# Kernel tuning notes

Hardware: AMD Instinct MI355X
Metric: run time of the kernel (lower is better)

The kernel has to match this reference:

```python
import jax, jax.numpy as jnp
import numpy as np

DT = 0.001  # euler step size (module default dt)
T = 2000    # num_timesteps
N_IN = 8192
N_OUT = 4096


def setup_inputs() -> dict:
    key = jax.random.key(0)
    k_x, k_w = jax.random.split(key)
    x = jax.random.normal(k_x, (T, N_IN), dtype=jnp.float32)
    # module initializes weight.data.uniform_(-0.1, 0.1)
    weight = jax.random.uniform(k_w, (N_OUT, N_IN), dtype=jnp.float32, minval=-0.1, maxval=0.1)
    ones = jnp.ones((N_OUT,), dtype=jnp.float32)
    # default_lif_parameters broadcast to per-neuron vectors (constant_lif_parameters)
    return {
        "x": x,
        "weight": weight,
        "v_th": ones * 75.0,
        "v_rest": ones * 50.0,
        "v_reset": ones * 30.0,
        "t_ref": ones * 0.001,
        "tau": ones * 2.0,
    }


def reference(x, weight, v_th, v_rest, v_reset, t_ref, tau):
    # lif_input[t] = x[t] @ weight.T  -> [T, N_OUT]
    lif_input = x @ weight.T

    def step(carry, inp):
        v, refrac = carry
        # leak toward v_rest
        v = v - DT * tau * (v - v_rest)
        # integrate input only when not refractory
        v = v + jnp.where(refrac == 0, inp, jnp.zeros_like(inp))
        # count down refractory period
        refrac = jnp.where(refrac > 0, refrac - DT, jnp.zeros_like(refrac))
        # heavyside spike
        spike = (v - v_th >= 0).astype(v.dtype)
        sb = spike > 0
        # reset: refractory period and membrane potential
        refrac = jnp.where(sb, t_ref, refrac)
        v = jnp.where(sb, v_reset, v)
        return (v, refrac), spike

    v0 = v_rest.astype(x.dtype)               # v[0] = v_rest
    refrac0 = jnp.zeros_like(v0)
    # torch loop runs i = 1 .. T-1 consuming lif_input[i]
    _, spikes = jax.lax.scan(step, (v0, refrac0), lif_input[1:])
    s0 = jnp.zeros((1, spikes.shape[1]), dtype=spikes.dtype)  # s[0] stays zero
    return jnp.concatenate([s0, spikes], axis=0)  # [T, N_OUT]
```

## Files before the change

kernel.cpp:

```cpp
#include <hip/hip_runtime.h>
#include <hip/hip_bf16.h>


#define T_STEPS 2000
#define NIN_K   8192
#define NOUT_N  4096
#define MPAD    2048

typedef __attribute__((ext_vector_type(8))) _Float16 half8;
typedef __attribute__((ext_vector_type(4))) float f32x4;

#define GLL16(g, l)                                                              \
    __builtin_amdgcn_global_load_lds(                                            \
        (const __attribute__((address_space(1))) void*)(g),                      \
        (__attribute__((address_space(3))) void*)(l), 16, 0, 0)

__global__ __launch_bounds__(256) void split_f32(const float* __restrict__ src,
                                                 _Float16* __restrict__ hi,
                                                 _Float16* __restrict__ lo,
                                                 size_t n_valid) {
    const size_t i8 = (size_t)(blockIdx.x * 256u + threadIdx.x) * 8;
    float vv[8];
    if (i8 < n_valid) {
        float4 v0 = *(const float4*)(src + i8);
        float4 v1 = *(const float4*)(src + i8 + 4);
        vv[0] = v0.x; vv[1] = v0.y; vv[2] = v0.z; vv[3] = v0.w;
        vv[4] = v1.x; vv[5] = v1.y; vv[6] = v1.z; vv[7] = v1.w;
    } else {
#pragma unroll
        for (int j = 0; j < 8; ++j) vv[j] = 0.f;
    }
    half8 h8, l8;
#pragma unroll
    for (int j = 0; j < 8; ++j) {
        _Float16 h = (_Float16)vv[j];
        float r = __fsub_rn(vv[j], (float)h);
        h8[j] = h;
        l8[j] = (_Float16)(r * 4096.0f);
    }
    *(half8*)(hi + i8) = h8;
    *(half8*)(lo + i8) = l8;
}

__global__ __launch_bounds__(256, 2) void gemm_f16x2(const _Float16* __restrict__ A0,
                                                     const _Float16* __restrict__ A1,
                                                     const _Float16* __restrict__ B0,
                                                     const _Float16* __restrict__ B1,
                                                     float* __restrict__ C) {
    __shared__ _Float16 lds[4][128 * 64];

    const int tid  = threadIdx.x;
    const int wave = tid >> 6;
    const int lane = tid & 63;
    const int bm = blockIdx.y * 128;
    const int bn = blockIdx.x * 128;
    const int wm = (wave >> 1) * 64;
    const int wn = (wave & 1) * 64;

    const int srow = tid >> 3;
    const int skswz = ((tid & 7) ^ (srow & 7)) * 8;

    f32x4 acc0[4][4], acc1[4][4];
#pragma unroll
    for (int i = 0; i < 4; ++i)
#pragma unroll
        for (int j = 0; j < 4; ++j) {
            acc0[i][j] = (f32x4){0.f, 0.f, 0.f, 0.f};
            acc1[i][j] = (f32x4){0.f, 0.f, 0.f, 0.f};
        }

    const int quad = lane >> 4;
    const int l16  = lane & 15;

    for (int k0 = 0; k0 < NIN_K; k0 += 64) {
        __syncthreads();
#pragma unroll
        for (int c = 0; c < 4; ++c) {
            const size_t ga = (size_t)(bm + c * 32 + srow) * NIN_K + k0 + skswz;
            const size_t gb = (size_t)(bn + c * 32 + srow) * NIN_K + k0 + skswz;
            const int base = (c * 32 + wave * 8) * 64;
            GLL16(A0 + ga, &lds[0][base]);
            GLL16(A1 + ga, &lds[1][base]);
            GLL16(B0 + gb, &lds[2][base]);
            GLL16(B1 + gb, &lds[3][base]);
        }
        __syncthreads();

#pragma unroll
        for (int ks = 0; ks < 2; ++ks) {
            half8 b0f[4], b1f[4];
#pragma unroll
            for (int j = 0; j < 4; ++j) {
                const int row = wn + j * 16 + l16;
                const int off = row * 64 + ((ks * 4 + quad) ^ (row & 7)) * 8;
                b0f[j] = *(const half8*)&lds[2][off];
                b1f[j] = *(const half8*)&lds[3][off];
            }
#pragma unroll
            for (int i = 0; i < 4; ++i) {
                const int row = wm + i * 16 + l16;
                const int off = row * 64 + ((ks * 4 + quad) ^ (row & 7)) * 8;
                const half8 a0f = *(const half8*)&lds[0][off];
                const half8 a1f = *(const half8*)&lds[1][off];
#pragma unroll
                for (int j = 0; j < 4; ++j) {
                    acc0[i][j] = __builtin_amdgcn_mfma_f32_16x16x32_f16(a0f, b0f[j], acc0[i][j], 0, 0, 0);
                    acc1[i][j] = __builtin_amdgcn_mfma_f32_16x16x32_f16(a0f, b1f[j], acc1[i][j], 0, 0, 0);
                    acc1[i][j] = __builtin_amdgcn_mfma_f32_16x16x32_f16(a1f, b0f[j], acc1[i][j], 0, 0, 0);
                }
            }
        }
    }

    const float s = 1.0f / 4096.0f;
#pragma unroll
    for (int i = 0; i < 4; ++i)
#pragma unroll
        for (int j = 0; j < 4; ++j) {
            const int m = bm + wm + i * 16 + quad * 4;
            const int n = bn + wn + j * 16 + l16;
            float* cp = C + (size_t)m * NOUT_N + n;
#pragma unroll
            for (int r = 0; r < 4; ++r)
                cp[(size_t)r * NOUT_N] = __fmaf_rn(acc1[i][j][r], s, acc0[i][j][r]);
        }
}

#define BM 64
#define BN 64
#define BK 16
#define PAD 4
__global__ __launch_bounds__(256) void gemm_bt(const float* __restrict__ A,
                                               const float* __restrict__ B,
                                               float* __restrict__ C,
                                               int M, int N, int K) {
    __shared__ float As[BK][BM + PAD];
    __shared__ float Bs[BK][BN + PAD];
    const int bm = blockIdx.y * BM, bn = blockIdx.x * BN;
    const int tid = threadIdx.x;
    const int tx = tid & 15, ty = tid >> 4;
    const int lrow = tid >> 2, lk = (tid & 3) * 4;
    float acc[4][4];
#pragma unroll
    for (int i = 0; i < 4; ++i)
#pragma unroll
        for (int j = 0; j < 4; ++j) acc[i][j] = 0.0f;
    for (int k0 = 0; k0 < K; k0 += BK) {
        const int am = bm + lrow;
        float4 av = (am < M) ? *(const float4*)(A + (size_t)am * K + k0 + lk)
                             : make_float4(0.f, 0.f, 0.f, 0.f);
        As[lk + 0][lrow] = av.x; As[lk + 1][lrow] = av.y;
        As[lk + 2][lrow] = av.z; As[lk + 3][lrow] = av.w;
        float4 bv = *(const float4*)(B + (size_t)(bn + lrow) * K + k0 + lk);
        Bs[lk + 0][lrow] = bv.x; Bs[lk + 1][lrow] = bv.y;
        Bs[lk + 2][lrow] = bv.z; Bs[lk + 3][lrow] = bv.w;
        __syncthreads();
#pragma unroll
        for (int k = 0; k < BK; ++k) {
            float a[4], b[4];
#pragma unroll
            for (int i = 0; i < 4; ++i) a[i] = As[k][ty * 4 + i];
#pragma unroll
            for (int j = 0; j < 4; ++j) b[j] = Bs[k][tx * 4 + j];
#pragma unroll
            for (int i = 0; i < 4; ++i)
#pragma unroll
                for (int j = 0; j < 4; ++j) acc[i][j] += a[i] * b[j];
        }
        __syncthreads();
    }
#pragma unroll
    for (int i = 0; i < 4; ++i) {
        const int m = bm + ty * 4 + i;
        if (m < M) {
            float* cp = C + (size_t)m * N + bn + tx * 4;
#pragma unroll
            for (int j = 0; j < 4; ++j) cp[j] = acc[i][j];
        }
    }
}

__global__ void zero_rows(float* __restrict__ p, size_t n) {
    const size_t i = (size_t)blockIdx.x * 256 + threadIdx.x;
    if (i < n) p[i] = 0.0f;
}

__global__ __launch_bounds__(64) void lif_scan(const float* __restrict__ inp,
                                               const float* __restrict__ v_th_p,
                                               const float* __restrict__ v_rest_p,
                                               const float* __restrict__ v_reset_p,
                                               const float* __restrict__ t_ref_p,
                                               const float* __restrict__ tau_p,
                                               float* __restrict__ out) {
    const int lane = threadIdx.x;
    const int j = blockIdx.x * 64 + lane;

    const float vth = v_th_p[j], vrest = v_rest_p[j], vres = v_reset_p[j];
    const float tref = t_ref_p[j];
    const float cleak = __fmul_rn(0.001f, tau_p[j]);
    float v = vrest, refrac = 0.0f;
    out[j] = 0.0f;

    const float* plv = inp + (size_t)1 * NOUT_N + j;
    float* pst = out + (size_t)1 * NOUT_N + j;

    float p00, p01, p02, p03, p04, p05, p06, p07, p08, p09, p10, p11, p12, p13, p14, p15;
    float p16, p17, p18, p19, p20, p21, p22, p23, p24, p25, p26, p27, p28, p29, p30, p31;

#define LDP(PD)                                                                   \
    asm volatile("global_load_dword %0, %1, off" : "=v"(PD) : "v"(plv) : "memory"); \
    plv += NOUT_N;

#define STEPA(PD, WSTR)                                                           \
    {                                                                             \
        asm volatile(WSTR : "+v"(PD)::"memory");                                  \
        const float in = PD;                                                      \
        const float dd = __fmul_rn(cleak, __fsub_rn(v, vrest));                   \
        v = __fsub_rn(v, dd);                                                     \
        v = (refrac == 0.0f) ? __fadd_rn(v, in) : v;                              \
        refrac = (refrac > 0.0f) ? (refrac - 0.001f) : 0.0f;                      \
        const bool s = (__fsub_rn(v, vth) >= 0.0f);                               \
        const float spk = s ? 1.0f : 0.0f;                                        \
        asm volatile("global_store_dword %0, %1, off" ::"v"(pst), "v"(spk)        \
                     : "memory");                                                 \
        pst += NOUT_N;                                                            \
        asm volatile("global_load_dword %0, %1, off" : "=v"(PD) : "v"(plv)        \
                     : "memory");                                                 \
        plv += NOUT_N;                                                            \
        refrac = s ? tref : refrac;                                               \
        v = s ? vres : v;                                                         \
    }

#define GROUP32(WSTR)                                                             \
    STEPA(p00, WSTR) STEPA(p01, WSTR) STEPA(p02, WSTR) STEPA(p03, WSTR)           \
    STEPA(p04, WSTR) STEPA(p05, WSTR) STEPA(p06, WSTR) STEPA(p07, WSTR)           \
    STEPA(p08, WSTR) STEPA(p09, WSTR) STEPA(p10, WSTR) STEPA(p11, WSTR)           \
    STEPA(p12, WSTR) STEPA(p13, WSTR) STEPA(p14, WSTR) STEPA(p15, WSTR)           \
    STEPA(p16, WSTR) STEPA(p17, WSTR) STEPA(p18, WSTR) STEPA(p19, WSTR)           \
    STEPA(p20, WSTR) STEPA(p21, WSTR) STEPA(p22, WSTR) STEPA(p23, WSTR)           \
    STEPA(p24, WSTR) STEPA(p25, WSTR) STEPA(p26, WSTR) STEPA(p27, WSTR)           \
    STEPA(p28, WSTR) STEPA(p29, WSTR) STEPA(p30, WSTR) STEPA(p31, WSTR)

#define TAILSTEP(PD)                                                              \
    {                                                                             \
        const float in = PD;                                                      \
        const float dd = __fmul_rn(cleak, __fsub_rn(v, vrest));                   \
        v = __fsub_rn(v, dd);                                                     \
        v = (refrac == 0.0f) ? __fadd_rn(v, in) : v;                              \
        refrac = (refrac > 0.0f) ? (refrac - 0.001f) : 0.0f;                      \
        const bool s = (__fsub_rn(v, vth) >= 0.0f);                               \
        *pst = s ? 1.0f : 0.0f;                                                   \
        pst += NOUT_N;                                                            \
        refrac = s ? tref : refrac;                                               \
        v = s ? vres : v;                                                         \
    }

    LDP(p00) LDP(p01) LDP(p02) LDP(p03) LDP(p04) LDP(p05) LDP(p06) LDP(p07)
    LDP(p08) LDP(p09) LDP(p10) LDP(p11) LDP(p12) LDP(p13) LDP(p14) LDP(p15)
    LDP(p16) LDP(p17) LDP(p18) LDP(p19) LDP(p20) LDP(p21) LDP(p22) LDP(p23)
    LDP(p24) LDP(p25) LDP(p26) LDP(p27) LDP(p28) LDP(p29) LDP(p30) LDP(p31)

    GROUP32("s_waitcnt vmcnt(31)")

#pragma unroll 1
    for (int g = 1; g < 62; ++g) {
        GROUP32("s_waitcnt vmcnt(62)")
    }

    asm volatile("s_waitcnt vmcnt(0)" ::: "memory");
    __builtin_amdgcn_sched_barrier(0);

    TAILSTEP(p00) TAILSTEP(p01) TAILSTEP(p02) TAILSTEP(p03) TAILSTEP(p04)
    TAILSTEP(p05) TAILSTEP(p06) TAILSTEP(p07) TAILSTEP(p08) TAILSTEP(p09)
    TAILSTEP(p10) TAILSTEP(p11) TAILSTEP(p12) TAILSTEP(p13) TAILSTEP(p14)

#undef LDP
#undef STEPA
#undef GROUP32
#undef TAILSTEP
}

extern "C" void kernel_launch(void* const* d_in, const int* in_sizes, int n_in,
                              void* d_out, int out_size, void* d_ws, size_t ws_size,
                              hipStream_t stream) {
    const float* x       = (const float*)d_in[0];
    const float* w       = (const float*)d_in[1];
    const float* v_th    = (const float*)d_in[2];
    const float* v_rest  = (const float*)d_in[3];
    const float* v_reset = (const float*)d_in[4];
    const float* t_ref   = (const float*)d_in[5];
    const float* tau     = (const float*)d_in[6];
    float* out = (float*)d_out;

    const size_t LIF_B = (size_t)MPAD * NOUT_N * 4;
    const size_t XS_B  = (size_t)MPAD * NIN_K * 2;
    const size_t WS_B  = (size_t)NOUT_N * NIN_K * 2;
    const size_t NEED  = LIF_B + 2 * XS_B + 2 * WS_B;

    char* ws = (char*)d_ws;
    float* lif = (float*)ws;

    if (ws_size >= NEED) {
        _Float16* x0 = (_Float16*)(ws + LIF_B);
        _Float16* x1 = (_Float16*)(ws + LIF_B + XS_B);
        _Float16* w0 = (_Float16*)(ws + LIF_B + 2 * XS_B);
        _Float16* w1 = (_Float16*)(ws + LIF_B + 2 * XS_B + WS_B);

        const size_t nx = (size_t)MPAD * NIN_K;
        split_f32<<<nx / 8 / 256, 256, 0, stream>>>(x, x0, x1,
                                                    (size_t)T_STEPS * NIN_K);
        const size_t nw = (size_t)NOUT_N * NIN_K;
        split_f32<<<nw / 8 / 256, 256, 0, stream>>>(w, w0, w1, nw);

        dim3 g(NOUT_N / 128, MPAD / 128);
        gemm_f16x2<<<g, 256, 0, stream>>>(x0, x1, w0, w1, lif);
    } else {
        dim3 g(NOUT_N / BN, (T_STEPS + BM - 1) / BM);
        gemm_bt<<<g, 256, 0, stream>>>(x, w, lif, T_STEPS, NOUT_N, NIN_K);
        const size_t padn = (size_t)(MPAD - T_STEPS) * NOUT_N;
        zero_rows<<<(padn + 255) / 256, 256, 0, stream>>>(lif + (size_t)T_STEPS * NOUT_N, padn);
    }

    lif_scan<<<NOUT_N / 64, 64, 0, stream>>>(lif, v_th, v_rest, v_reset, t_ref, tau, out);
}
```

Baseline: 693.6 us.

## Double-buffer LDS in split-f16 GEMM and move to 8 waves per block

The split-fp16 GEMM now uses two LDS buffers so the global-to-LDS loads for the next K tile are issued while MFMAs run on the current one. Synchronisation uses explicit vmcnt waits and raw barriers instead of two __syncthreads per step. The block grows to 512 threads, each wave covering a 64x32 sub-tile, which halves the accumulator registers per wave. LDS use doubles to 128KB per block, which may limit blocks per CU, and the hand-written vmcnt counts must match the load ordering for the results to stay correct.

```diff
diff --git a/kernel.cpp b/kernel.cpp
--- a/kernel.cpp
+++ b/kernel.cpp
@@ -42,29 +42,41 @@
     *(half8*)(lo + i8) = l8;
 }
 
-__global__ __launch_bounds__(256, 2) void gemm_f16x2(const _Float16* __restrict__ A0,
+__global__ __launch_bounds__(512, 2) void gemm_f16x2(const _Float16* __restrict__ A0,
                                                      const _Float16* __restrict__ A1,
                                                      const _Float16* __restrict__ B0,
                                                      const _Float16* __restrict__ B1,
                                                      float* __restrict__ C) {
-    __shared__ _Float16 lds[4][128 * 64];
+    __shared__ _Float16 lds[2][4][128 * 64];
 
     const int tid  = threadIdx.x;
     const int wave = tid >> 6;
     const int lane = tid & 63;
     const int bm = blockIdx.y * 128;
     const int bn = blockIdx.x * 128;
-    const int wm = (wave >> 1) * 64;
-    const int wn = (wave & 1) * 64;
-
-    const int srow = tid >> 3;
-    const int skswz = ((tid & 7) ^ (srow & 7)) * 8;
-
-    f32x4 acc0[4][4], acc1[4][4];
+    const int wm = (wave >> 2) * 64;
+    const int wn = (wave & 3) * 32;
+
+    const int sr0 = wave * 16 + (lane >> 3);
+    const int sr1 = sr0 + 8;
+    const int sc0 = ((lane & 7) ^ (sr0 & 7)) * 8;
+    const int sc1 = ((lane & 7) ^ (sr1 & 7)) * 8;
+    const _Float16* pa00 = A0 + (size_t)(bm + sr0) * NIN_K + sc0;
+    const _Float16* pa01 = A0 + (size_t)(bm + sr1) * NIN_K + sc1;
+    const _Float16* pa10 = A1 + (size_t)(bm + sr0) * NIN_K + sc0;
+    const _Float16* pa11 = A1 + (size_t)(bm + sr1) * NIN_K + sc1;
+    const _Float16* pb00 = B0 + (size_t)(bn + sr0) * NIN_K + sc0;
+    const _Float16* pb01 = B0 + (size_t)(bn + sr1) * NIN_K + sc1;
+    const _Float16* pb10 = B1 + (size_t)(bn + sr0) * NIN_K + sc0;
+    const _Float16* pb11 = B1 + (size_t)(bn + sr1) * NIN_K + sc1;
+    const int ldsOff0 = (wave * 16) * 64;
+    const int ldsOff1 = (wave * 16 + 8) * 64;
+
+    f32x4 acc0[4][2], acc1[4][2];
 #pragma unroll
     for (int i = 0; i < 4; ++i)
 #pragma unroll
-        for (int j = 0; j < 4; ++j) {
+        for (int j = 0; j < 2; ++j) {
             acc0[i][j] = (f32x4){0.f, 0.f, 0.f, 0.f};
             acc1[i][j] = (f32x4){0.f, 0.f, 0.f, 0.f};
         }
@@ -72,51 +84,80 @@
     const int quad = lane >> 4;
     const int l16  = lane & 15;
 
-    for (int k0 = 0; k0 < NIN_K; k0 += 64) {
-        __syncthreads();
-#pragma unroll
-        for (int c = 0; c < 4; ++c) {
-            const size_t ga = (size_t)(bm + c * 32 + srow) * NIN_K + k0 + skswz;
-            const size_t gb = (size_t)(bn + c * 32 + srow) * NIN_K + k0 + skswz;
-            const int base = (c * 32 + wave * 8) * 64;
-            GLL16(A0 + ga, &lds[0][base]);
-            GLL16(A1 + ga, &lds[1][base]);
-            GLL16(B0 + gb, &lds[2][base]);
-            GLL16(B1 + gb, &lds[3][base]);
-        }
-        __syncthreads();
-
-#pragma unroll
-        for (int ks = 0; ks < 2; ++ks) {
-            half8 b0f[4], b1f[4];
-#pragma unroll
-            for (int j = 0; j < 4; ++j) {
-                const int row = wn + j * 16 + l16;
-                const int off = row * 64 + ((ks * 4 + quad) ^ (row & 7)) * 8;
-                b0f[j] = *(const half8*)&lds[2][off];
-                b1f[j] = *(const half8*)&lds[3][off];
-            }
-#pragma unroll
-            for (int i = 0; i < 4; ++i) {
-                const int row = wm + i * 16 + l16;
-                const int off = row * 64 + ((ks * 4 + quad) ^ (row & 7)) * 8;
-                const half8 a0f = *(const half8*)&lds[0][off];
-                const half8 a1f = *(const half8*)&lds[1][off];
-#pragma unroll
-                for (int j = 0; j < 4; ++j) {
-                    acc0[i][j] = __builtin_amdgcn_mfma_f32_16x16x32_f16(a0f, b0f[j], acc0[i][j], 0, 0, 0);
-                    acc1[i][j] = __builtin_amdgcn_mfma_f32_16x16x32_f16(a0f, b1f[j], acc1[i][j], 0, 0, 0);
-                    acc1[i][j] = __builtin_amdgcn_mfma_f32_16x16x32_f16(a1f, b0f[j], acc1[i][j], 0, 0, 0);
-                }
-            }
-        }
-    }
+#define STAGE(BUF)                                                               \
+    {                                                                            \
+        GLL16(pa00, &lds[BUF][0][ldsOff0]); GLL16(pa01, &lds[BUF][0][ldsOff1]);  \
+        GLL16(pa10, &lds[BUF][1][ldsOff0]); GLL16(pa11, &lds[BUF][1][ldsOff1]);  \
+        GLL16(pb00, &lds[BUF][2][ldsOff0]); GLL16(pb01, &lds[BUF][2][ldsOff1]);  \
+        GLL16(pb10, &lds[BUF][3][ldsOff0]); GLL16(pb11, &lds[BUF][3][ldsOff1]);  \
+        pa00 += 64; pa01 += 64; pa10 += 64; pa11 += 64;                          \
+        pb00 += 64; pb01 += 64; pb10 += 64; pb11 += 64;                          \
+    }
+
+#define WAIT8  asm volatile("s_waitcnt vmcnt(8)" ::: "memory")
+#define WAIT0  asm volatile("s_waitcnt vmcnt(0)" ::: "memory")
+#define BARRIER                                                                  \
+    {                                                                            \
+        __builtin_amdgcn_s_barrier();                                            \
+        __builtin_amdgcn_sched_barrier(0);                                       \
+    }
+
+#define COMPUTE(BUF)                                                             \
+    _Pragma("unroll") for (int ks = 0; ks < 2; ++ks) {                           \
+        half8 b0f[2], b1f[2];                                                    \
+        _Pragma("unroll") for (int j = 0; j < 2; ++j) {                          \
+            const int row = wn + j * 16 + l16;                                   \
+            const int off = row * 64 + ((ks * 4 + quad) ^ (row & 7)) * 8;        \
+            b0f[j] = *(const half8*)&lds[BUF][2][off];                           \
+            b1f[j] = *(const half8*)&lds[BUF][3][off];                           \
+        }                                                                        \
+        _Pragma("unroll") for (int i = 0; i < 4; ++i) {                          \
+            const int row = wm + i * 16 + l16;                                   \
+            const int off = row * 64 + ((ks * 4 + quad) ^ (row & 7)) * 8;        \
+            const half8 a0f = *(const half8*)&lds[BUF][0][off];                  \
+            const half8 a1f = *(const half8*)&lds[BUF][1][off];                  \
+            _Pragma("unroll") for (int j = 0; j < 2; ++j) {                      \
+                acc0[i][j] = __builtin_amdgcn_mfma_f32_16x16x32_f16(a0f, b0f[j], acc0[i][j], 0, 0, 0); \
+                acc1[i][j] = __builtin_amdgcn_mfma_f32_16x16x32_f16(a0f, b1f[j], acc1[i][j], 0, 0, 0); \
+                acc1[i][j] = __builtin_amdgcn_mfma_f32_16x16x32_f16(a1f, b0f[j], acc1[i][j], 0, 0, 0); \
+            }                                                                    \
+        }                                                                        \
+    }
+
+    STAGE(0)
+
+#pragma unroll 1
+    for (int t = 0; t < 126; t += 2) {
+        STAGE(1)
+        WAIT8;
+        BARRIER
+        COMPUTE(0)
+        BARRIER
+        STAGE(0)
+        WAIT8;
+        BARRIER
+        COMPUTE(1)
+        BARRIER
+    }
+    STAGE(1)
+    WAIT8;
+    BARRIER
+    COMPUTE(0)
+    WAIT0;
+    BARRIER
+    COMPUTE(1)
+
+#undef STAGE
+#undef WAIT8
+#undef WAIT0
+#undef BARRIER
+#undef COMPUTE
 
     const float s = 1.0f / 4096.0f;
 #pragma unroll
     for (int i = 0; i < 4; ++i)
 #pragma unroll
-        for (int j = 0; j < 4; ++j) {
+        for (int j = 0; j < 2; ++j) {
             const int m = bm + wm + i * 16 + quad * 4;
             const int n = bn + wn + j * 16 + l16;
             float* cp = C + (size_t)m * NOUT_N + n;
@@ -313,7 +354,7 @@
         split_f32<<<nw / 8 / 256, 256, 0, stream>>>(w, w0, w1, nw);
 
         dim3 g(NOUT_N / 128, MPAD / 128);
-        gemm_f16x2<<<g, 256, 0, stream>>>(x0, x1, w0, w1, lif);
+        gemm_f16x2<<<g, 512, 0, stream>>>(x0, x1, w0, w1, lif);
     } else {
         dim3 g(NOUT_N / BN, (T_STEPS + BM - 1) / BM);
         gemm_bt<<<g, 256, 0, stream>>>(x, w, lif, T_STEPS, NOUT_N, NIN_K);
```

Result: slower. 733.7 us (+5.8%).
